# Kernel optimization log

Hardware: AMD Instinct MI355X
Metric: run time of the kernel (lower is better)

Reference implementation:

```python
import jax, jax.numpy as jnp
import numpy as np

D_MODEL = 1024
D_INNER = 4096
K = 127
B, L = 2, 4096

def setup_inputs() -> dict:
    key = jax.random.key(0)
    k1, k2, k3, k4, k5 = jax.random.split(key, 5)
    x = jax.random.normal(k1, (B, L, D_MODEL), dtype=jnp.float32)
    # in_proj: Linear(d, 2*m) -> weight [2m, d] (torch convention)
    w_in = jax.random.normal(k2, (2 * D_INNER, D_MODEL), dtype=jnp.float32) * (1.0 / np.sqrt(D_MODEL))
    # depthwise conv weight: [m, 1, k] in torch; store as [m, k]
    w_dw = jax.random.normal(k3, (D_INNER, K), dtype=jnp.float32) * (1.0 / np.sqrt(K))
    b_dw = jax.random.normal(k4, (D_INNER,), dtype=jnp.float32) * 0.01
    # out_proj: Linear(m, d) -> weight [d, m]
    w_out = jax.random.normal(k5, (D_MODEL, D_INNER), dtype=jnp.float32) * (1.0 / np.sqrt(D_INNER))
    return {"x": x, "w_in": w_in, "w_dw": w_dw, "b_dw": b_dw, "w_out": w_out}

def _causal_dwconv(v, w_dw, b_dw):
    # v: [B, L, m]; causal depthwise conv with kernel K
    # pad K-1 on the left only (equivalent to torch pad=K-1 then [..., :L])
    v_bcl = jnp.transpose(v, (0, 2, 1))  # [B, m, L]
    out = jax.lax.conv_general_dilated(
        v_bcl,
        w_dw[:, None, :],  # [m, 1, K]
        window_strides=(1,),
        padding=[(K - 1, 0)],
        feature_group_count=D_INNER,
        dimension_numbers=("NCH", "OIH", "NCH"),
    )
    out = out + b_dw[None, :, None]
    return jnp.transpose(out, (0, 2, 1))  # [B, L, m]

def reference(x, w_in, w_dw, b_dw, w_out):
    vg = jnp.einsum("bld,ed->ble", x, w_in)  # [B, L, 2m]
    v, g = jnp.split(vg, 2, axis=-1)
    v = _causal_dwconv(v, w_dw, b_dw)
    y = jax.nn.silu(v) * jax.nn.silu(g)
    return jnp.einsum("blm,dm->bld", y, w_out)
```

## Files before the change

### kernel.cpp

```cpp
#include <hip/hip_runtime.h>
#include <hip/hip_bf16.h>
#include <cstdint>
#include <cstddef>

typedef __bf16 bf16_t;
typedef __attribute__((ext_vector_type(8))) __bf16 bf16x8;
typedef __attribute__((ext_vector_type(4))) __bf16 bf16x4;
typedef __attribute__((ext_vector_type(4))) float floatx4;

__device__ __forceinline__ void async_copy_16B(const void* g, void* l) {
  __builtin_amdgcn_global_load_lds(
      (const __attribute__((address_space(1))) void*)g,
      (__attribute__((address_space(3))) void*)l, 16, 0, 0);
}

__global__ __launch_bounds__(256) void prep(
    const float* __restrict__ x, const float* __restrict__ w_in,
    const float* __restrict__ w_out, const float* __restrict__ w_dw,
    bf16_t* __restrict__ x_bf, bf16_t* __restrict__ wi_bf,
    bf16_t* __restrict__ wo_bf, float* __restrict__ wt) {
  const int tid = blockIdx.x * 256 + threadIdx.x;
  if (tid < 5242880) {
    const float* src;
    bf16_t* dst;
    int off;
    if (tid < 2097152) {
      src = x; dst = x_bf; off = tid;
    } else if (tid < 4194304) {
      src = w_in; dst = wi_bf; off = tid - 2097152;
    } else {
      src = w_out; dst = wo_bf; off = tid - 4194304;
    }
    const float4 v = *(const float4*)(src + (size_t)off * 4);
    bf16x4 o;
    o.x = (bf16_t)v.x; o.y = (bf16_t)v.y; o.z = (bf16_t)v.z; o.w = (bf16_t)v.w;
    *(bf16x4*)(dst + (size_t)off * 4) = o;
  } else {
    const int idx = tid - 5242880;
    if (idx < 127 * 4096) {
      const int j = idx >> 12;
      const int c = idx & 4095;
      wt[idx] = w_dw[c * 127 + j];
    }
  }
}

template <int BN_, typename OutT>
__global__ __launch_bounds__(256) void gemm_bt64(
    const bf16_t* __restrict__ A, const bf16_t* __restrict__ B,
    OutT* __restrict__ C, int M, int N, int K) {
  constexpr int BM_ = 128;
  constexpr int FI = (BN_ == 128) ? 4 : 2;
  constexpr int FJ = 4;
  constexpr int ACH = BM_ * 8;
  constexpr int CH = (BM_ + BN_) * 8;
  constexpr int CPT = CH / 256;

  __shared__ bf16_t smem[(BM_ + BN_) * 64];
  bf16_t* const As0 = smem;
  bf16_t* const As1 = smem + BM_ * 32;
  bf16_t* const Bs0 = smem + BM_ * 64;
  bf16_t* const Bs1 = smem + BM_ * 64 + BN_ * 32;

  const int t = threadIdx.x;
  const int lane = t & 63;
  const int wave = t >> 6;
  const int m0 = blockIdx.y * BM_;
  const int n0 = blockIdx.x * BN_;
  const int wr = (BN_ == 128) ? (wave >> 1) * 64 : wave * 32;
  const int wc = (BN_ == 128) ? (wave & 1) * 64 : 0;
  const int fr = lane & 15;
  const int fk = (lane >> 4) * 8;

  floatx4 acc[FI][FJ] = {};

  const int kTiles = K / 64;
  for (int kt = 0; kt < kTiles; ++kt) {
    const int k0 = kt * 64;
    __syncthreads();
#pragma unroll
    for (int it = 0; it < CPT; ++it) {
      const int p = it * 256 + t;
      const bf16_t* gsrc;
      if (p < BM_ * 4) {
        const int row = p >> 2, kc = (p & 3) * 8;
        gsrc = A + (size_t)(m0 + row) * K + k0 + kc;
      } else if (p < ACH) {
        const int q = p - BM_ * 4;
        const int row = q >> 2, kc = 32 + (q & 3) * 8;
        gsrc = A + (size_t)(m0 + row) * K + k0 + kc;
      } else if (p < ACH + BN_ * 4) {
        const int q = p - ACH;
        const int row = q >> 2, kc = (q & 3) * 8;
        gsrc = B + (size_t)(n0 + row) * K + k0 + kc;
      } else {
        const int q = p - ACH - BN_ * 4;
        const int row = q >> 2, kc = 32 + (q & 3) * 8;
        gsrc = B + (size_t)(n0 + row) * K + k0 + kc;
      }
      async_copy_16B(gsrc, smem + p * 8);
    }
    __syncthreads();

    bf16x8 af[FI][2], bfr[FJ][2];
#pragma unroll
    for (int i = 0; i < FI; ++i) {
      const int r = (wr + i * 16 + fr) * 32 + fk;
      af[i][0] = *(const bf16x8*)(As0 + r);
      af[i][1] = *(const bf16x8*)(As1 + r);
    }
#pragma unroll
    for (int j = 0; j < FJ; ++j) {
      const int r = (wc + j * 16 + fr) * 32 + fk;
      bfr[j][0] = *(const bf16x8*)(Bs0 + r);
      bfr[j][1] = *(const bf16x8*)(Bs1 + r);
    }
#pragma unroll
    for (int h = 0; h < 2; ++h)
#pragma unroll
      for (int i = 0; i < FI; ++i)
#pragma unroll
        for (int j = 0; j < FJ; ++j)
          acc[i][j] = __builtin_amdgcn_mfma_f32_16x16x32_bf16(
              af[i][h], bfr[j][h], acc[i][j], 0, 0, 0);
  }

  const int cr = (lane >> 4) * 4;
  const int cc = lane & 15;
#pragma unroll
  for (int i = 0; i < FI; ++i)
#pragma unroll
    for (int j = 0; j < FJ; ++j)
#pragma unroll
      for (int r = 0; r < 4; ++r) {
        const int row = m0 + wr + i * 16 + cr + r;
        const int col = n0 + wc + j * 16 + cc;
        C[(size_t)row * N + col] = (OutT)acc[i][j][r];
      }
}

#define CONV_L 128
#define CROWS 254

__global__ __launch_bounds__(256) void conv_gate(
    const bf16_t* __restrict__ vg, const float* __restrict__ wt,
    const float* __restrict__ b_dw, bf16_t* __restrict__ y) {
  __shared__ bf16_t vt[CROWS * 64];
  const int t = threadIdx.x;
  const int lane = t & 63;
  const int wave = t >> 6;
  const int c0 = blockIdx.x * 64;
  const int lt = blockIdx.y & 31;
  const int b = blockIdx.y >> 5;
  const int l0 = lt * CONV_L;

  for (int chunk = t; chunk < CROWS * 8; chunk += 256) {
    const int row = chunk >> 3;
    const int cc = (chunk & 7) * 8;
    const int l = l0 - 126 + row;
    uint4* dst = (uint4*)(vt + row * 64 + cc);
    if (l < 0) {
      *dst = make_uint4(0u, 0u, 0u, 0u);
    } else {
      *dst = *(const uint4*)(vg + (size_t)(b * 4096 + l) * 8192 + c0 + cc);
    }
  }
  __syncthreads();

  const int c = c0 + lane;
  const int r0 = wave * 32;
  const float bias = b_dw[c];
  float acc[32], win[32];
#pragma unroll
  for (int i = 0; i < 32; ++i) acc[i] = bias;
#pragma unroll
  for (int i = 0; i < 32; ++i) win[i] = (float)vt[(r0 + i) * 64 + lane];

  const float* wcp = wt + c;
#pragma unroll 1
  for (int jo = 0; jo < 96; jo += 32) {
#pragma unroll
    for (int ji = 0; ji < 32; ++ji) {
      const int j = jo + ji;
      const float wj = wcp[(size_t)j * 4096];
#pragma unroll
      for (int i = 0; i < 32; ++i) acc[i] += wj * win[(ji + i) & 31];
      win[ji] = (float)vt[(r0 + 32 + j) * 64 + lane];
    }
  }
#pragma unroll
  for (int ji = 0; ji < 31; ++ji) {
    const int j = 96 + ji;
    const float wj = wcp[(size_t)j * 4096];
#pragma unroll
    for (int i = 0; i < 32; ++i) acc[i] += wj * win[(ji + i) & 31];
    if (ji < 30) win[ji] = (float)vt[(r0 + 32 + j) * 64 + lane];
  }

  const int lb = l0 + r0;
  const bf16_t* gp = vg + (size_t)(b * 4096 + lb) * 8192 + 4096 + c;
  bf16_t* yp = y + (size_t)(b * 4096 + lb) * 4096 + c;
#pragma unroll
  for (int i = 0; i < 32; ++i) {
    const float gv = (float)gp[(size_t)i * 8192];
    const float v = acc[i];
    const float sv = v / (1.f + __expf(-v));
    const float sg = gv / (1.f + __expf(-gv));
    yp[(size_t)i * 4096] = (bf16_t)(sv * sg);
  }
}

extern "C" void kernel_launch(void* const* d_in, const int* in_sizes, int n_in,
                              void* d_out, int out_size, void* d_ws,
                              size_t ws_size, hipStream_t stream) {
  const float* x     = (const float*)d_in[0];
  const float* w_in  = (const float*)d_in[1];
  const float* w_dw  = (const float*)d_in[2];
  const float* b_dw  = (const float*)d_in[3];
  const float* w_out = (const float*)d_in[4];
  float* out = (float*)d_out;

  char* p = (char*)d_ws;
  bf16_t* x_bf  = (bf16_t*)p; p += (size_t)8192 * 1024 * 2;
  bf16_t* wi_bf = (bf16_t*)p; p += (size_t)8192 * 1024 * 2;
  bf16_t* wo_bf = (bf16_t*)p; p += (size_t)1024 * 4096 * 2;
  float*  wt    = (float*)p;  p += (size_t)127 * 4096 * 4;
  bf16_t* vg    = (bf16_t*)p; p += (size_t)8192 * 8192 * 2;
  bf16_t* y     = (bf16_t*)p; p += (size_t)8192 * 4096 * 2;

  prep<<<22512, 256, 0, stream>>>(x, w_in, w_out, w_dw, x_bf, wi_bf, wo_bf, wt);

  gemm_bt64<128, bf16_t><<<dim3(64, 64), 256, 0, stream>>>(x_bf, wi_bf, vg,
                                                           8192, 8192, 1024);
  conv_gate<<<dim3(64, 64), 256, 0, stream>>>(vg, wt, b_dw, y);
  gemm_bt64<64, float><<<dim3(16, 64), 256, 0, stream>>>(y, wo_bf, out,
                                                         8192, 1024, 4096);
}
```

Baseline: 501.6 us.

## Switch pipeline to fp16 and compute depthwise conv with packed fdot2

Changes all intermediate storage and the MFMA GEMMs from bf16 to fp16. The causal depthwise conv moves from scalar fp32 FMAs to packed half2 dot products (fdot2): the weights are pre-paired into half2 taps and the inputs are kept in a ring of half2 pairs, which halves the FMA instruction count in the conv. This trades bf16 dynamic range for fp16 precision, and carries overflow risk if activations exceed the fp16 range. Odd and even output rows use shifted weight pairings, including a zero-padded extra tap.

```diff
diff --git a/kernel.cpp b/kernel.cpp
--- a/kernel.cpp
+++ b/kernel.cpp
@@ -3,9 +3,10 @@
 #include <cstdint>
 #include <cstddef>
 
-typedef __bf16 bf16_t;
-typedef __attribute__((ext_vector_type(8))) __bf16 bf16x8;
-typedef __attribute__((ext_vector_type(4))) __bf16 bf16x4;
+typedef __fp16 f16_t;
+typedef __attribute__((ext_vector_type(8))) __fp16 f16x8;
+typedef __attribute__((ext_vector_type(4))) __fp16 f16x4;
+typedef __attribute__((ext_vector_type(2))) __fp16 h2_t;
 typedef __attribute__((ext_vector_type(4))) float floatx4;
 
 __device__ __forceinline__ void async_copy_16B(const void* g, void* l) {
@@ -17,37 +18,47 @@
 __global__ __launch_bounds__(256) void prep(
     const float* __restrict__ x, const float* __restrict__ w_in,
     const float* __restrict__ w_out, const float* __restrict__ w_dw,
-    bf16_t* __restrict__ x_bf, bf16_t* __restrict__ wi_bf,
-    bf16_t* __restrict__ wo_bf, float* __restrict__ wt) {
+    f16_t* __restrict__ x_h, f16_t* __restrict__ wi_h,
+    f16_t* __restrict__ wo_h, h2_t* __restrict__ wp) {
   const int tid = blockIdx.x * 256 + threadIdx.x;
   if (tid < 5242880) {
     const float* src;
-    bf16_t* dst;
+    f16_t* dst;
     int off;
     if (tid < 2097152) {
-      src = x; dst = x_bf; off = tid;
+      src = x; dst = x_h; off = tid;
     } else if (tid < 4194304) {
-      src = w_in; dst = wi_bf; off = tid - 2097152;
+      src = w_in; dst = wi_h; off = tid - 2097152;
     } else {
-      src = w_out; dst = wo_bf; off = tid - 4194304;
+      src = w_out; dst = wo_h; off = tid - 4194304;
     }
     const float4 v = *(const float4*)(src + (size_t)off * 4);
-    bf16x4 o;
-    o.x = (bf16_t)v.x; o.y = (bf16_t)v.y; o.z = (bf16_t)v.z; o.w = (bf16_t)v.w;
-    *(bf16x4*)(dst + (size_t)off * 4) = o;
+    f16x4 o;
+    o.x = (f16_t)v.x; o.y = (f16_t)v.y; o.z = (f16_t)v.z; o.w = (f16_t)v.w;
+    *(f16x4*)(dst + (size_t)off * 4) = o;
   } else {
     const int idx = tid - 5242880;
-    if (idx < 127 * 4096) {
-      const int j = idx >> 12;
+    if (idx < 128 * 4096) {
+      const int p = idx >> 12;
       const int c = idx & 4095;
-      wt[idx] = w_dw[c * 127 + j];
+      float a, b;
+      if (p < 126) {
+        a = w_dw[c * 127 + p]; b = w_dw[c * 127 + p + 1];
+      } else if (p == 126) {
+        a = w_dw[c * 127 + 126]; b = 0.f;
+      } else {
+        a = 0.f; b = w_dw[c * 127 + 0];
+      }
+      h2_t w;
+      w.x = (f16_t)a; w.y = (f16_t)b;
+      wp[idx] = w;
     }
   }
 }
 
 template <int BN_, typename OutT>
 __global__ __launch_bounds__(256) void gemm_bt64(
-    const bf16_t* __restrict__ A, const bf16_t* __restrict__ B,
+    const f16_t* __restrict__ A, const f16_t* __restrict__ B,
     OutT* __restrict__ C, int M, int N, int K) {
   constexpr int BM_ = 128;
   constexpr int FI = (BN_ == 128) ? 4 : 2;
@@ -56,11 +67,11 @@
   constexpr int CH = (BM_ + BN_) * 8;
   constexpr int CPT = CH / 256;
 
-  __shared__ bf16_t smem[(BM_ + BN_) * 64];
-  bf16_t* const As0 = smem;
-  bf16_t* const As1 = smem + BM_ * 32;
-  bf16_t* const Bs0 = smem + BM_ * 64;
-  bf16_t* const Bs1 = smem + BM_ * 64 + BN_ * 32;
+  __shared__ f16_t smem[(BM_ + BN_) * 64];
+  f16_t* const As0 = smem;
+  f16_t* const As1 = smem + BM_ * 32;
+  f16_t* const Bs0 = smem + BM_ * 64;
+  f16_t* const Bs1 = smem + BM_ * 64 + BN_ * 32;
 
   const int t = threadIdx.x;
   const int lane = t & 63;
@@ -81,7 +92,7 @@
 #pragma unroll
     for (int it = 0; it < CPT; ++it) {
       const int p = it * 256 + t;
-      const bf16_t* gsrc;
+      const f16_t* gsrc;
       if (p < BM_ * 4) {
         const int row = p >> 2, kc = (p & 3) * 8;
         gsrc = A + (size_t)(m0 + row) * K + k0 + kc;
@@ -102,18 +113,18 @@
     }
     __syncthreads();
 
-    bf16x8 af[FI][2], bfr[FJ][2];
+    f16x8 af[FI][2], bfr[FJ][2];
 #pragma unroll
     for (int i = 0; i < FI; ++i) {
       const int r = (wr + i * 16 + fr) * 32 + fk;
-      af[i][0] = *(const bf16x8*)(As0 + r);
-      af[i][1] = *(const bf16x8*)(As1 + r);
+      af[i][0] = *(const f16x8*)(As0 + r);
+      af[i][1] = *(const f16x8*)(As1 + r);
     }
 #pragma unroll
     for (int j = 0; j < FJ; ++j) {
       const int r = (wc + j * 16 + fr) * 32 + fk;
-      bfr[j][0] = *(const bf16x8*)(Bs0 + r);
-      bfr[j][1] = *(const bf16x8*)(Bs1 + r);
+      bfr[j][0] = *(const f16x8*)(Bs0 + r);
+      bfr[j][1] = *(const f16x8*)(Bs1 + r);
     }
 #pragma unroll
     for (int h = 0; h < 2; ++h)
@@ -121,7 +132,7 @@
       for (int i = 0; i < FI; ++i)
 #pragma unroll
         for (int j = 0; j < FJ; ++j)
-          acc[i][j] = __builtin_amdgcn_mfma_f32_16x16x32_bf16(
+          acc[i][j] = __builtin_amdgcn_mfma_f32_16x16x32_f16(
               af[i][h], bfr[j][h], acc[i][j], 0, 0, 0);
   }
 
@@ -143,9 +154,9 @@
 #define CROWS 254
 
 __global__ __launch_bounds__(256) void conv_gate(
-    const bf16_t* __restrict__ vg, const float* __restrict__ wt,
-    const float* __restrict__ b_dw, bf16_t* __restrict__ y) {
-  __shared__ bf16_t vt[CROWS * 64];
+    const f16_t* __restrict__ vg, const h2_t* __restrict__ wp,
+    const float* __restrict__ b_dw, f16_t* __restrict__ y) {
+  __shared__ f16_t vt[CROWS * 64];
   const int t = threadIdx.x;
   const int lane = t & 63;
   const int wave = t >> 6;
@@ -170,43 +181,60 @@
   const int c = c0 + lane;
   const int r0 = wave * 32;
   const float bias = b_dw[c];
-  float acc[32], win[32];
+  float acc[32];
 #pragma unroll
   for (int i = 0; i < 32; ++i) acc[i] = bias;
-#pragma unroll
-  for (int i = 0; i < 32; ++i) win[i] = (float)vt[(r0 + i) * 64 + lane];
-
-  const float* wcp = wt + c;
-#pragma unroll 1
-  for (int jo = 0; jo < 96; jo += 32) {
-#pragma unroll
-    for (int ji = 0; ji < 32; ++ji) {
-      const int j = jo + ji;
-      const float wj = wcp[(size_t)j * 4096];
-#pragma unroll
-      for (int i = 0; i < 32; ++i) acc[i] += wj * win[(ji + i) & 31];
-      win[ji] = (float)vt[(r0 + 32 + j) * 64 + lane];
-    }
-  }
-#pragma unroll
-  for (int ji = 0; ji < 31; ++ji) {
-    const int j = 96 + ji;
-    const float wj = wcp[(size_t)j * 4096];
-#pragma unroll
-    for (int i = 0; i < 32; ++i) acc[i] += wj * win[(ji + i) & 31];
-    if (ji < 30) win[ji] = (float)vt[(r0 + 32 + j) * 64 + lane];
+
+  h2_t ring[17];
+#pragma unroll
+  for (int m = 0; m < 17; ++m) {
+    h2_t pr;
+    pr.x = vt[(r0 + 2 * m) * 64 + lane];
+    pr.y = vt[(r0 + 2 * m + 1) * 64 + lane];
+    ring[m] = pr;
+  }
+
+  const h2_t* wpc = wp + c;
+  {
+    const h2_t w0 = wpc[127 * 4096];
+#pragma unroll
+    for (int h = 0; h < 16; ++h)
+      acc[2 * h + 1] =
+          __builtin_amdgcn_fdot2(w0, ring[h], acc[2 * h + 1], false);
+  }
+
+#pragma unroll
+  for (int k = 0; k < 64; ++k) {
+    const h2_t we = wpc[(size_t)(2 * k) * 4096];
+#pragma unroll
+    for (int h = 0; h < 16; ++h)
+      acc[2 * h] =
+          __builtin_amdgcn_fdot2(we, ring[(k + h) % 17], acc[2 * h], false);
+    if (k < 63) {
+      const h2_t wo = wpc[(size_t)(2 * k + 1) * 4096];
+#pragma unroll
+      for (int h = 0; h < 16; ++h)
+        acc[2 * h + 1] = __builtin_amdgcn_fdot2(wo, ring[(k + 1 + h) % 17],
+                                                acc[2 * h + 1], false);
+      if (k < 62) {
+        h2_t np;
+        np.x = vt[(r0 + 2 * k + 34) * 64 + lane];
+        np.y = vt[(r0 + 2 * k + 35) * 64 + lane];
+        ring[k % 17] = np;
+      }
+    }
   }
 
   const int lb = l0 + r0;
-  const bf16_t* gp = vg + (size_t)(b * 4096 + lb) * 8192 + 4096 + c;
-  bf16_t* yp = y + (size_t)(b * 4096 + lb) * 4096 + c;
+  const f16_t* gp = vg + (size_t)(b * 4096 + lb) * 8192 + 4096 + c;
+  f16_t* yp = y + (size_t)(b * 4096 + lb) * 4096 + c;
 #pragma unroll
   for (int i = 0; i < 32; ++i) {
     const float gv = (float)gp[(size_t)i * 8192];
     const float v = acc[i];
     const float sv = v / (1.f + __expf(-v));
     const float sg = gv / (1.f + __expf(-gv));
-    yp[(size_t)i * 4096] = (bf16_t)(sv * sg);
+    yp[(size_t)i * 4096] = (f16_t)(sv * sg);
   }
 }
 
@@ -221,18 +249,18 @@
   float* out = (float*)d_out;
 
   char* p = (char*)d_ws;
-  bf16_t* x_bf  = (bf16_t*)p; p += (size_t)8192 * 1024 * 2;
-  bf16_t* wi_bf = (bf16_t*)p; p += (size_t)8192 * 1024 * 2;
-  bf16_t* wo_bf = (bf16_t*)p; p += (size_t)1024 * 4096 * 2;
-  float*  wt    = (float*)p;  p += (size_t)127 * 4096 * 4;
-  bf16_t* vg    = (bf16_t*)p; p += (size_t)8192 * 8192 * 2;
-  bf16_t* y     = (bf16_t*)p; p += (size_t)8192 * 4096 * 2;
-
-  prep<<<22512, 256, 0, stream>>>(x, w_in, w_out, w_dw, x_bf, wi_bf, wo_bf, wt);
-
-  gemm_bt64<128, bf16_t><<<dim3(64, 64), 256, 0, stream>>>(x_bf, wi_bf, vg,
-                                                           8192, 8192, 1024);
-  conv_gate<<<dim3(64, 64), 256, 0, stream>>>(vg, wt, b_dw, y);
-  gemm_bt64<64, float><<<dim3(16, 64), 256, 0, stream>>>(y, wo_bf, out,
+  f16_t* x_h  = (f16_t*)p; p += (size_t)8192 * 1024 * 2;
+  f16_t* wi_h = (f16_t*)p; p += (size_t)8192 * 1024 * 2;
+  f16_t* wo_h = (f16_t*)p; p += (size_t)1024 * 4096 * 2;
+  h2_t*  wp   = (h2_t*)p;  p += (size_t)128 * 4096 * 4;
+  f16_t* vg   = (f16_t*)p; p += (size_t)8192 * 8192 * 2;
+  f16_t* y    = (f16_t*)p; p += (size_t)8192 * 4096 * 2;
+
+  prep<<<22528, 256, 0, stream>>>(x, w_in, w_out, w_dw, x_h, wi_h, wo_h, wp);
+
+  gemm_bt64<128, f16_t><<<dim3(64, 64), 256, 0, stream>>>(x_h, wi_h, vg,
+                                                          8192, 8192, 1024);
+  conv_gate<<<dim3(64, 64), 256, 0, stream>>>(vg, wp, b_dw, y);
+  gemm_bt64<64, float><<<dim3(16, 64), 256, 0, stream>>>(y, wo_h, out,
                                                          8192, 1024, 4096);
 }
```

New measurement: 585.5 us. 1.17x slower.
